# Performance work log

Measured on AMD Instinct MI355X. Metric: run time of the kernel, lower is better.

## Reference

```python
import jax, jax.numpy as jnp
import numpy as np
from functools import partial

MAX_SPAN_WIDTH = 8


def setup_inputs() -> dict:
    key = jax.random.key(0)
    ks = jax.random.split(key, 8)
    B, S, H = 4, 256, 256
    NE, D = 50000, 256  # entity_embedding_dim == hidden_size
    inp = {
        "embeddings": jax.random.normal(ks[0], (B, S, H), jnp.float32),          # BERT outputs[0]
        "entity_table": jax.random.normal(ks[1], (NE, D), jnp.float32) * 0.02,   # nn.Embedding weight
        "span_W": jax.random.normal(ks[2], (2 * H + 1, H), jnp.float32) * 0.02,  # span_embedding Linear
        "span_b": jax.random.normal(ks[3], (H,), jnp.float32) * 0.02,
        "gcn_W1": jax.random.normal(ks[4], (D, H), jnp.float32) * 0.02,
        "gcn_b1": jax.random.normal(ks[5], (H,), jnp.float32) * 0.02,
        "gcn_W2": jax.random.normal(ks[6], (H, H), jnp.float32) * 0.02,
        "gcn_b2": jax.random.normal(ks[7], (H,), jnp.float32) * 0.02,
        "k": 8,
    }
    return inp


def _star_adj_norm(k, dtype):
    # k-node star graph (node 0 hub) with self-loops, symmetric GCN normalization
    A = jnp.zeros((k, k), dtype).at[0, 1:].set(1.0).at[1:, 0].set(1.0) + jnp.eye(k, dtype=dtype)
    deg = A.sum(axis=1)
    return A / jnp.sqrt(deg[:, None] * deg[None, :])


def reference(embeddings, entity_table, span_W, span_b, gcn_W1, gcn_b1, gcn_W2, gcn_b2, k):
    B, S, H = embeddings.shape
    Wmax = MAX_SPAN_WIDTH
    dtype = embeddings.dtype

    # token_inputs: CLS embedding per example
    cls = embeddings[:, 0, :]  # [B, H]

    # Vectorized ragged span max-pool: running max over widths 1..Wmax.
    # span_max[w, b, s, :] = max(embeddings[b, s : s+w+1, :])
    neg_inf = jnp.array(-jnp.inf, dtype)
    maxes = []
    cur = embeddings
    maxes.append(cur)
    for w in range(1, Wmax):
        shifted = jnp.concatenate(
            [embeddings[:, w:, :], jnp.full((B, w, H), neg_inf, dtype)], axis=1)
        cur = jnp.maximum(cur, shifted)  # -inf pad => out-of-range positions ignored
        maxes.append(cur)
    span_max = jnp.stack(maxes, axis=0)  # [Wmax, B, S, H]

    # concat(max-pool, CLS, span width) -> span_embedding Linear
    cls_b = jnp.broadcast_to(cls[None, :, None, :], (Wmax, B, S, H))
    width_feat = jnp.broadcast_to(
        jnp.arange(1, Wmax + 1, dtype=dtype)[:, None, None, None], (Wmax, B, S, 1))
    span_inputs = jnp.concatenate([span_max, cls_b, width_feat], axis=-1)  # [Wmax,B,S,2H+1]
    span_inputs = span_inputs.reshape(Wmax * B * S, 2 * H + 1)             # [N, 2H+1]
    span_repr = span_inputs @ span_W + span_b                              # [N, H]

    # build_subgraph: top-k similar entities per span (memory-bound similarity + top-k)
    sims = span_repr @ entity_table.T          # [N, NE]  ~1.6GB intermediate
    _, topk_idx = jax.lax.top_k(sims, k)       # [N, k]
    node_x = entity_table[topk_idx]            # gather -> [N, k, D]

    # 2-layer GCN on the fixed star subgraph (gather-linear-scatter equivalent)
    A_norm = _star_adj_norm(k, dtype)          # [k, k]
    h = jax.nn.relu(jnp.einsum('ij,njd,dh->nih', A_norm, node_x, gcn_W1) + gcn_b1)
    subgraph_out = jnp.einsum('ij,njd,dh->nih', A_norm, h, gcn_W2) + gcn_b2  # [N, k, H]

    return cls, span_repr, subgraph_out
```

## Files before the change

### kernel.cpp

```cpp
#include <hip/hip_runtime.h>

typedef unsigned short u16;
typedef unsigned int   u32;
typedef unsigned long long u64;
typedef short bf16x8 __attribute__((ext_vector_type(8)));
typedef float f32x4  __attribute__((ext_vector_type(4)));

#define INF_F __builtin_inff()

__device__ __forceinline__ u16 f2bf(float f) {
  u32 u = __float_as_uint(f);
  return (u16)((u + 0x7FFFu + ((u >> 16) & 1u)) >> 16);
}

__device__ __forceinline__ u32 sortf(float f) {
  u32 u = __float_as_uint(f);
  return u ^ ((u32)((int)u >> 31) | 0x80000000u);
}
__device__ __forceinline__ float unsortf(u32 s) {
  u32 u = s ^ ((s & 0x80000000u) ? 0x80000000u : 0xFFFFFFFFu);
  return __uint_as_float(u);
}
__device__ __forceinline__ u64 sx64(u64 v, int m) {
  u32 lo = __shfl_xor((u32)v, m);
  u32 hi = __shfl_xor((u32)(v >> 32), m);
  return ((u64)hi << 32) | lo;
}

__device__ __forceinline__ void gload_lds16(const void* g, void* l) {
  __builtin_amdgcn_global_load_lds(
      (const __attribute__((address_space(1))) u32*)g,
      (__attribute__((address_space(3))) u32*)l, 16, 0, 0);
}

__global__ __launch_bounds__(256) void k0_cvt(
    const float* __restrict__ src, u16* __restrict__ dst, int n4) {
  int id = blockIdx.x * 256 + threadIdx.x;
  if (id >= n4) return;
  float4 v = ((const float4*)src)[id];
  ((ushort4*)dst)[id] = make_ushort4(f2bf(v.x), f2bf(v.y), f2bf(v.z), f2bf(v.w));
}

__global__ __launch_bounds__(256) void k1_span(
    const float* __restrict__ emb, const float* __restrict__ Wsp,
    const float* __restrict__ bsp,
    float* __restrict__ out0, float* __restrict__ out1,
    u16* __restrict__ spanbf) {
  __shared__ float SM[8][256];
  __shared__ float CLS[256];
  const int bid = blockIdx.x;
  const int b = bid >> 8, s = bid & 255;
  const int t = threadIdx.x;
  const float* eb = emb + (size_t)b * 65536;

  CLS[t] = eb[t];
  if (s == 0) out0[b * 256 + t] = eb[t];

  float m = eb[s * 256 + t];
  SM[0][t] = m;
  #pragma unroll
  for (int w = 1; w < 8; ++w) {
    if (s + w < 256) m = fmaxf(m, eb[(s + w) * 256 + t]);
    SM[w][t] = m;
  }
  __syncthreads();

  float cc = 0.f;
  for (int k = 0; k < 256; k += 4) {
    float4 cq = *(const float4*)&CLS[k];
    cc += cq.x * Wsp[(size_t)(256 + k + 0) * 256 + t];
    cc += cq.y * Wsp[(size_t)(256 + k + 1) * 256 + t];
    cc += cq.z * Wsp[(size_t)(256 + k + 2) * 256 + t];
    cc += cq.w * Wsp[(size_t)(256 + k + 3) * 256 + t];
  }
  float acc[8];
  const float base = bsp[t] + cc;
  #pragma unroll
  for (int w = 0; w < 8; ++w) acc[w] = base;

  for (int k = 0; k < 256; k += 4) {
    float w0 = Wsp[(size_t)(k + 0) * 256 + t];
    float w1 = Wsp[(size_t)(k + 1) * 256 + t];
    float w2 = Wsp[(size_t)(k + 2) * 256 + t];
    float w3 = Wsp[(size_t)(k + 3) * 256 + t];
    #pragma unroll
    for (int w = 0; w < 8; ++w) {
      float4 smq = *(const float4*)&SM[w][k];
      acc[w] += smq.x * w0; acc[w] += smq.y * w1;
      acc[w] += smq.z * w2; acc[w] += smq.w * w3;
    }
  }
  const float wm = Wsp[(size_t)512 * 256 + t];
  #pragma unroll
  for (int w = 0; w < 8; ++w) {
    float val = acc[w] + (float)(w + 1) * wm;
    size_t idx = ((size_t)w * 1024 + bid) * 256 + t;
    out1[idx] = val;
    spanbf[idx] = f2bf(val);
  }
}

__global__ __launch_bounds__(128) void k2_mfma(
    const u16* __restrict__ spanbf, const u16* __restrict__ entbf, int ne,
    float* __restrict__ Rpv, int* __restrict__ Rpi) {
  __shared__ u32 Elds[8192];
  __shared__ u64 Q[2][64][17];
  const int t = threadIdx.x, lane = t & 63, wv = t >> 6;
  const int m = lane & 15, q = lane >> 4, q4 = q * 4;
  const int p = blockIdx.x & 7, rg = blockIdx.x >> 3;
  const int psz = (ne + 7) >> 3;
  const int e_start = p * psz;
  const int e_end = min(ne, e_start + psz);
  const int rowbase = rg * 128 + wv * 64;
  const u64 gm = 0xFFFFull << (q * 16);
  const u64 lanelow = (lane == 63) ? 0x7FFFFFFFFFFFFFFFull
                                   : ((1ull << (lane + 1)) - 1) >> 1;
  const u64 gml = gm & lanelow;
  const int row = lane & 15;
  const int ls5 = lane >> 5;

  const u64 KINIT = ((u64)sortf(-INF_F) << 32);
  u64 slot[4][4];
  float myth[4], th[4][4];
  #pragma unroll
  for (int h = 0; h < 4; ++h) {
    myth[h] = -INF_F;
    #pragma unroll
    for (int s = 0; s < 4; ++s) { slot[h][s] = KINIT; th[h][s] = -INF_F; }
  }

  bf16x8 a[4][8];
  #pragma unroll
  for (int h = 0; h < 4; ++h)
    #pragma unroll
    for (int s = 0; s < 8; ++s)
      a[h][s] = *(const bf16x8*)(spanbf
                  + (size_t)(rowbase + h * 16 + m) * 256 + s * 32 + q * 8);

  auto issue = [&](int c, int ebase) {
    #pragma unroll
    for (int i = 0; i < 4; ++i) {
      int e = c * 16 + wv * 8 + i * 2 + ls5;
      int ge = min(ebase + e, e_end - 1);
      int xoff = ((lane & 31) ^ (e & 31)) << 4;
      const char* src = (const char*)entbf + (size_t)ge * 512 + xoff;
      char* dst = (char*)Elds + (c << 13) + (wv << 12) + (i << 10);
      gload_lds16(src, dst);
    }
  };

  const int ntiles = (e_end - e_start + 63) >> 6;
  #pragma unroll
  for (int c = 0; c < 4; ++c) issue(c, e_start);

  for (int tile = 0; tile < ntiles; ++tile) {
    const int eb = e_start + (tile << 6);
    const int ebn = eb + 64;
    const bool notlast = (tile + 1 < ntiles);
    #pragma unroll
    for (int c = 0; c < 4; ++c) {
      if (notlast) asm volatile("s_waitcnt vmcnt(12)" ::: "memory");
      else         asm volatile("s_waitcnt vmcnt(0)"  ::: "memory");
      __builtin_amdgcn_sched_barrier(0);
      __builtin_amdgcn_s_barrier();

      f32x4 acc[4];
      #pragma unroll
      for (int h = 0; h < 4; ++h) acc[h] = (f32x4){0.f, 0.f, 0.f, 0.f};
      const int el = c * 16 + m, sw = el & 31, bc = el << 5;
      #pragma unroll
      for (int s = 0; s < 8; ++s) {
        int qq = s * 4 + q;
        bf16x8 bfr = *(const bf16x8*)((const char*)Elds + ((bc | (qq ^ sw)) << 4));
        #pragma unroll
        for (int h = 0; h < 4; ++h)
          acc[h] = __builtin_amdgcn_mfma_f32_16x16x32_bf16(a[h][s], bfr, acc[h], 0, 0, 0);
      }
      const int gent = eb + c * 16 + m;
      const bool valid = gent < e_end;

      #pragma unroll
      for (int h = 0; h < 4; ++h) {
        bool any = valid & ((acc[h][0] > th[h][0]) | (acc[h][1] > th[h][1]) |
                            (acc[h][2] > th[h][2]) | (acc[h][3] > th[h][3]));
        if (!__ballot(any)) continue;
        u64 M[4];
        #pragma unroll
        for (int r = 0; r < 4; ++r) {
          bool hr = valid && (acc[h][r] > th[h][r]);
          M[r] = __ballot(hr);
          if (hr) {
            int pos = (int)__popcll(M[r] & gml);
            Q[wv][h * 16 + q4 + r][pos] =
                ((u64)sortf(acc[h][r]) << 32) | (u32)(~(u32)gent);
          }
        }
        u64 msk = (row & 2) ? ((row & 1) ? M[3] : M[2])
                            : ((row & 1) ? M[1] : M[0]);
        int cnt = (int)__popcll((msk >> ((row >> 2) << 4)) & 0xFFFFull);
        int cmax = cnt;
        #pragma unroll
        for (int o = 1; o < 16; o <<= 1)
          cmax = max(cmax, __shfl_xor(cmax, o));
        for (int j = 0; j < cmax; ++j) {
          u64 cand = Q[wv][h * 16 + row][j];
          if (j >= cnt) cand = 0;
          u64 m01 = slot[h][0] < slot[h][1] ? slot[h][0] : slot[h][1];
          u64 m23 = slot[h][2] < slot[h][3] ? slot[h][2] : slot[h][3];
          u64 lmin = m01 < m23 ? m01 : m23;
          u64 g = sx64(lmin, 16); if (g < lmin) lmin = g;
          g = sx64(lmin, 32); u64 gmin = (g < lmin) ? g : lmin;
          bool ins = cand > gmin;
          #pragma unroll
          for (int s2 = 0; s2 < 4; ++s2)
            if (ins && slot[h][s2] == gmin) slot[h][s2] = cand;
        }
        {
          u64 m01 = slot[h][0] < slot[h][1] ? slot[h][0] : slot[h][1];
          u64 m23 = slot[h][2] < slot[h][3] ? slot[h][2] : slot[h][3];
          u64 lmin = m01 < m23 ? m01 : m23;
          u64 g = sx64(lmin, 16); if (g < lmin) lmin = g;
          g = sx64(lmin, 32); if (g < lmin) lmin = g;
          myth[h] = unsortf((u32)(lmin >> 32));
          #pragma unroll
          for (int r = 0; r < 4; ++r) th[h][r] = __shfl(myth[h], q4 + r);
        }
      }

      __builtin_amdgcn_s_barrier();
      if (notlast) issue(c, ebn);
    }
  }

  {
    const int sg = lane >> 4;
    #pragma unroll
    for (int h = 0; h < 4; ++h) {
      int r0 = rowbase + h * 16 + row;
      #pragma unroll
      for (int s = 0; s < 4; ++s) {
        u64 e0 = slot[h][s];
        int col = p * 16 + sg * 4 + s;
        Rpv[(size_t)r0 * 128 + col] = unsortf((u32)(e0 >> 32));
        Rpi[(size_t)r0 * 128 + col] = (int)(~(u32)e0);
      }
    }
  }
}

__global__ __launch_bounds__(256) void k2_merge(
    const float* __restrict__ Rpv, const int* __restrict__ Rpi,
    int* __restrict__ Ridx) {
  const int t = threadIdx.x, lane = t & 63, wv = t >> 6;
  const int row = blockIdx.x * 4 + wv;
  const float va = Rpv[(size_t)row * 128 + lane];
  const int   ea = Rpi[(size_t)row * 128 + lane];
  const float vb = Rpv[(size_t)row * 128 + 64 + lane];
  const int   eb = Rpi[(size_t)row * 128 + 64 + lane];
  int ca = 0, cb = 0;
  for (int i = 0; i < 64; ++i) {
    float ov = __shfl(va, i); int oi = __shfl(ea, i);
    ca += (ov > va || (ov == va && oi < ea));
    cb += (ov > vb || (ov == vb && oi < eb));
  }
  for (int i = 0; i < 64; ++i) {
    float ov = __shfl(vb, i); int oi = __shfl(eb, i);
    ca += (ov > va || (ov == va && oi < ea));
    cb += (ov > vb || (ov == vb && oi < eb));
  }
  if (ca < 16) Ridx[(size_t)row * 16 + ca] = ea;
  if (cb < 16) Ridx[(size_t)row * 16 + cb] = eb;
}

__global__ __launch_bounds__(256, 3) void k3_gcn(
    const float* __restrict__ out1, const float* __restrict__ ent,
    const int* __restrict__ Ridx,
    const float* __restrict__ W1, const float* __restrict__ b1,
    const float* __restrict__ W2, const float* __restrict__ b2,
    float* __restrict__ out2, int ne) {
  __shared__ __align__(16) char UN[34560];
  __shared__ __align__(16) u16 Abf[32][272];
  __shared__ int cidx[4][16];
  __shared__ int chos[4][8];
  const int t = threadIdx.x;
  const int lane = t & 63, wv = t >> 6;
  const int m = lane & 15, q = lane >> 4;
  const int n0 = blockIdx.x * 4;

  {
    float  (*SPR)[256] = (float (*)[256])UN;
    double (*dpart)[4] = (double (*)[4])(UN + 4096);
    double (*sims)[16] = (double (*)[16])(UN + 6144);
    #pragma unroll
    for (int g = 0; g < 4; ++g)
      SPR[g][t] = out1[(size_t)(n0 + g) * 256 + t];
    if (t < 64) {
      int g = t >> 4, j = t & 15;
      int c = Ridx[(size_t)(n0 + g) * 16 + j];
      if ((unsigned)c >= (unsigned)ne) c = 0;
      cidx[g][j] = c;
    }
    __syncthreads();

    {
      const int pr = t >> 2, sub = t & 3;
      const int g = pr >> 4, j = pr & 15;
      const float* er = ent + (size_t)cidx[g][j] * 256 + sub * 64;
      const float* sr = &SPR[g][sub * 64];
      double s = 0.0;
      #pragma unroll
      for (int i = 0; i < 64; i += 4) {
        float4 e4 = *(const float4*)&er[i];
        float4 s4 = *(const float4*)&sr[i];
        s += (double)e4.x * (double)s4.x;
        s += (double)e4.y * (double)s4.y;
        s += (double)e4.z * (double)s4.z;
        s += (double)e4.w * (double)s4.w;
      }
      dpart[pr][sub] = s;
    }
    __syncthreads();
    if (t < 64) {
      int g = t >> 4, j = t & 15;
      sims[g][j] = dpart[t][0] + dpart[t][1] + dpart[t][2] + dpart[t][3];
    }
    __syncthreads();
    if (t < 4) {
      unsigned used = 0;
      for (int o = 0; o < 8; ++o) {
        int best = -1; double bv = 0.0; int bi = 0;
        for (int j = 0; j < 16; ++j) {
          if (used & (1u << j)) continue;
          if (best < 0 || sims[t][j] > bv || (sims[t][j] == bv && cidx[t][j] < bi)) {
            best = j; bv = sims[t][j]; bi = cidx[t][j];
          }
        }
        used |= (1u << best);
        chos[t][o] = cidx[t][best];
      }
    }
    __syncthreads();
  }

  {
    const int r = t >> 3, cb = t & 7;
    const float* src = ent + (size_t)chos[r >> 3][r & 7] * 256 + cb * 32;
    u32 pk[16];
    #pragma unroll
    for (int i = 0; i < 8; ++i) {
      float4 v = *(const float4*)&src[i * 4];
      pk[2 * i]     = (u32)f2bf(v.x) | ((u32)f2bf(v.y) << 16);
      pk[2 * i + 1] = (u32)f2bf(v.z) | ((u32)f2bf(v.w) << 16);
    }
    uint4* dst = (uint4*)&Abf[r][cb * 32];
    #pragma unroll
    for (int i = 0; i < 4; ++i)
      dst[i] = make_uint4(pk[4 * i], pk[4 * i + 1], pk[4 * i + 2], pk[4 * i + 3]);
  }

  auto run_gemm = [&](const float* __restrict__ Wg) {
    f32x4 acc[2][4];
    #pragma unroll
    for (int mt = 0; mt < 2; ++mt)
      #pragma unroll
      for (int nt = 0; nt < 4; ++nt)
        acc[mt][nt] = (f32x4){0.f, 0.f, 0.f, 0.f};

    for (int s = 0; s < 8; ++s) {
      __syncthreads();
      {
        const float* src = Wg + (size_t)(s * 32) * 256 + t;
        u32 pk[16];
        #pragma unroll
        for (int i = 0; i < 16; ++i) {
          float lo = src[(size_t)(2 * i) * 256];
          float hi = src[(size_t)(2 * i + 1) * 256];
          pk[i] = (u32)f2bf(lo) | ((u32)f2bf(hi) << 16);
        }
        uint4* dst = (uint4*)(UN + t * 80);
        #pragma unroll
        for (int i = 0; i < 4; ++i)
          dst[i] = make_uint4(pk[4 * i], pk[4 * i + 1], pk[4 * i + 2], pk[4 * i + 3]);
      }
      __syncthreads();
      #pragma unroll
      for (int mt = 0; mt < 2; ++mt) {
        bf16x8 af = *(const bf16x8*)((const char*)Abf
                       + (mt * 16 + m) * 544 + s * 64 + q * 16);
        #pragma unroll
        for (int nt = 0; nt < 4; ++nt) {
          const int col = wv * 64 + nt * 16 + m;
          bf16x8 bf = *(const bf16x8*)(UN + col * 80 + q * 16);
          acc[mt][nt] = __builtin_amdgcn_mfma_f32_16x16x32_bf16(
              af, bf, acc[mt][nt], 0, 0, 0);
        }
      }
    }
    __syncthreads();
    #pragma unroll
    for (int mt = 0; mt < 2; ++mt)
      #pragma unroll
      for (int nt = 0; nt < 4; ++nt)
        #pragma unroll
        for (int r = 0; r < 4; ++r)
          *(float*)(UN + (((mt * 16 + q * 4 + r) * 268)
                          + (wv * 64 + nt * 16 + m)) * 4) = acc[mt][nt][r];
    __syncthreads();
  };

  run_gemm(W1);
  {
    const float bb = b1[t];
    #pragma unroll
    for (int g = 0; g < 4; ++g) {
      float v[8];
      #pragma unroll
      for (int j = 0; j < 8; ++j)
        v[j] = *(const float*)(UN + ((g * 8 + j) * 268 + t) * 4);
      float ssum = 0.f;
      #pragma unroll
      for (int j = 1; j < 8; ++j) ssum += v[j];
      Abf[g * 8][t] = f2bf(fmaxf(v[0] * 0.125f + ssum * 0.25f + bb, 0.f));
      #pragma unroll
      for (int j = 1; j < 8; ++j)
        Abf[g * 8 + j][t] = f2bf(fmaxf(v[0] * 0.25f + v[j] * 0.5f + bb, 0.f));
    }
  }

  run_gemm(W2);
  {
    const float bb = b2[t];
    #pragma unroll
    for (int g = 0; g < 4; ++g) {
      float v[8];
      #pragma unroll
      for (int j = 0; j < 8; ++j)
        v[j] = *(const float*)(UN + ((g * 8 + j) * 268 + t) * 4);
      float ssum = 0.f;
      #pragma unroll
      for (int j = 1; j < 8; ++j) ssum += v[j];
      float* ob = out2 + (size_t)(n0 + g) * 2048 + t;
      ob[0] = v[0] * 0.125f + ssum * 0.25f + bb;
      #pragma unroll
      for (int j = 1; j < 8; ++j)
        ob[(size_t)j * 256] = v[0] * 0.25f + v[j] * 0.5f + bb;
    }
  }
}

extern "C" void kernel_launch(void* const* d_in, const int* in_sizes, int n_in,
                              void* d_out, int out_size, void* d_ws, size_t ws_size,
                              hipStream_t stream) {
  const float* emb = (const float*)d_in[0];
  const float* ent = (const float*)d_in[1];
  const float* Wsp = (const float*)d_in[2];
  const float* bsp = (const float*)d_in[3];
  const float* W1  = (const float*)d_in[4];
  const float* b1  = (const float*)d_in[5];
  const float* W2  = (const float*)d_in[6];
  const float* b2  = (const float*)d_in[7];
  const int ne = in_sizes[1] / 256;

  float* out  = (float*)d_out;
  float* out0 = out;
  float* out1 = out + 1024;
  float* out2 = out + 1024 + 2097152;

  char* ov = (char*)out2;
  u16*   entbf  = (u16*)(ov);
  u16*   spanbf = (u16*)(ov + 33554432);
  float* Rpv    = (float*)(ov + 41943040);
  int*   Rpi    = (int*)  (ov + 50331648);
  int*   Ridx   = (int*)d_ws;

  hipLaunchKernelGGL(k0_cvt, dim3((ne * 64 + 255) / 256), dim3(256), 0, stream,
                     ent, entbf, ne * 64);
  hipLaunchKernelGGL(k1_span, dim3(1024), dim3(256), 0, stream,
                     emb, Wsp, bsp, out0, out1, spanbf);
  hipLaunchKernelGGL(k2_mfma, dim3(512), dim3(128), 0, stream,
                     spanbf, entbf, ne, Rpv, Rpi);
  hipLaunchKernelGGL(k2_merge, dim3(2048), dim3(256), 0, stream,
                     Rpv, Rpi, Ridx);
  hipLaunchKernelGGL(k3_gcn, dim3(2048), dim3(256), 0, stream,
                     out1, ent, Ridx, W1, b1, W2, b2, out2, ne);
}
```

Baseline: 883.1 us.

## Split entity range 16-way and use 3-slot rolling chunk pipeline in top-k kernel

Doubles the entity partitions per row group (16 instead of 8), launching 1024 blocks so more waves run concurrently on the GPU, and the merge kernel now merges 256 partial candidates per row. The load pipeline changes from 4-chunk tiles with a trailing barrier to a 3-slot rolling buffer that prefetches one chunk ahead, shrinking LDS use to allow 2 blocks per CU. The candidate queue padding is replaced with XOR swizzling to avoid bank conflicts. It adds merge work, plus extra partial-result traffic and slot-maintenance overhead per partition.

```diff
diff --git a/kernel.cpp b/kernel.cpp
--- a/kernel.cpp
+++ b/kernel.cpp
@@ -100,15 +100,15 @@
   }
 }
 
-__global__ __launch_bounds__(128) void k2_mfma(
+__global__ __launch_bounds__(128, 2) void k2_mfma(
     const u16* __restrict__ spanbf, const u16* __restrict__ entbf, int ne,
     float* __restrict__ Rpv, int* __restrict__ Rpi) {
-  __shared__ u32 Elds[8192];
-  __shared__ u64 Q[2][64][17];
+  __shared__ u32 Elds[6144];
+  __shared__ u64 Q[2][64][16];
   const int t = threadIdx.x, lane = t & 63, wv = t >> 6;
   const int m = lane & 15, q = lane >> 4, q4 = q * 4;
-  const int p = blockIdx.x & 7, rg = blockIdx.x >> 3;
-  const int psz = (ne + 7) >> 3;
+  const int p = blockIdx.x & 15, rg = blockIdx.x >> 4;
+  const int psz = (ne + 15) >> 4;
   const int e_start = p * psz;
   const int e_end = min(ne, e_start + psz);
   const int rowbase = rg * 128 + wv * 64;
@@ -137,99 +137,97 @@
       a[h][s] = *(const bf16x8*)(spanbf
                   + (size_t)(rowbase + h * 16 + m) * 256 + s * 32 + q * 8);
 
-  auto issue = [&](int c, int ebase) {
+  auto issue = [&](int k, int sl) {
+    const int cb = e_start + (k << 4);
     #pragma unroll
     for (int i = 0; i < 4; ++i) {
-      int e = c * 16 + wv * 8 + i * 2 + ls5;
-      int ge = min(ebase + e, e_end - 1);
+      int eo = wv * 8 + i * 2 + ls5;
+      int e  = (sl << 4) + eo;
+      int ge = min(cb + eo, e_end - 1);
       int xoff = ((lane & 31) ^ (e & 31)) << 4;
-      const char* src = (const char*)entbf + (size_t)ge * 512 + xoff;
-      char* dst = (char*)Elds + (c << 13) + (wv << 12) + (i << 10);
-      gload_lds16(src, dst);
+      gload_lds16((const char*)entbf + (size_t)ge * 512 + xoff,
+                  (char*)Elds + (sl << 13) + (wv << 12) + (i << 10));
     }
   };
 
-  const int ntiles = (e_end - e_start + 63) >> 6;
-  #pragma unroll
-  for (int c = 0; c < 4; ++c) issue(c, e_start);
-
-  for (int tile = 0; tile < ntiles; ++tile) {
-    const int eb = e_start + (tile << 6);
-    const int ebn = eb + 64;
-    const bool notlast = (tile + 1 < ntiles);
-    #pragma unroll
-    for (int c = 0; c < 4; ++c) {
-      if (notlast) asm volatile("s_waitcnt vmcnt(12)" ::: "memory");
-      else         asm volatile("s_waitcnt vmcnt(0)"  ::: "memory");
-      __builtin_amdgcn_sched_barrier(0);
-      __builtin_amdgcn_s_barrier();
-
-      f32x4 acc[4];
-      #pragma unroll
-      for (int h = 0; h < 4; ++h) acc[h] = (f32x4){0.f, 0.f, 0.f, 0.f};
-      const int el = c * 16 + m, sw = el & 31, bc = el << 5;
-      #pragma unroll
-      for (int s = 0; s < 8; ++s) {
-        int qq = s * 4 + q;
-        bf16x8 bfr = *(const bf16x8*)((const char*)Elds + ((bc | (qq ^ sw)) << 4));
-        #pragma unroll
-        for (int h = 0; h < 4; ++h)
-          acc[h] = __builtin_amdgcn_mfma_f32_16x16x32_bf16(a[h][s], bfr, acc[h], 0, 0, 0);
-      }
-      const int gent = eb + c * 16 + m;
-      const bool valid = gent < e_end;
-
-      #pragma unroll
-      for (int h = 0; h < 4; ++h) {
-        bool any = valid & ((acc[h][0] > th[h][0]) | (acc[h][1] > th[h][1]) |
-                            (acc[h][2] > th[h][2]) | (acc[h][3] > th[h][3]));
-        if (!__ballot(any)) continue;
-        u64 M[4];
-        #pragma unroll
-        for (int r = 0; r < 4; ++r) {
-          bool hr = valid && (acc[h][r] > th[h][r]);
-          M[r] = __ballot(hr);
-          if (hr) {
-            int pos = (int)__popcll(M[r] & gml);
-            Q[wv][h * 16 + q4 + r][pos] =
-                ((u64)sortf(acc[h][r]) << 32) | (u32)(~(u32)gent);
-          }
+  const int nch = (e_end - e_start + 15) >> 4;
+  int cs = 0;
+  issue(0, 0);
+
+  for (int pc = 0; pc < nch; ++pc) {
+    int is_ = cs + 1; if (is_ == 3) is_ = 0;
+    if (pc + 1 < nch) {
+      issue(pc + 1, is_);
+      asm volatile("s_waitcnt vmcnt(4)" ::: "memory");
+    } else {
+      asm volatile("s_waitcnt vmcnt(0)" ::: "memory");
+    }
+    __builtin_amdgcn_sched_barrier(0);
+    __builtin_amdgcn_s_barrier();
+
+    f32x4 acc[4];
+    #pragma unroll
+    for (int h = 0; h < 4; ++h) acc[h] = (f32x4){0.f, 0.f, 0.f, 0.f};
+    const int el = (cs << 4) + m, sw = el & 31, bc = el << 5;
+    #pragma unroll
+    for (int s = 0; s < 8; ++s) {
+      int qq = s * 4 + q;
+      bf16x8 bfr = *(const bf16x8*)((const char*)Elds + ((bc | (qq ^ sw)) << 4));
+      #pragma unroll
+      for (int h = 0; h < 4; ++h)
+        acc[h] = __builtin_amdgcn_mfma_f32_16x16x32_bf16(a[h][s], bfr, acc[h], 0, 0, 0);
+    }
+    const int gent = e_start + (pc << 4) + m;
+    const bool valid = gent < e_end;
+
+    #pragma unroll
+    for (int h = 0; h < 4; ++h) {
+      bool any = valid & ((acc[h][0] > th[h][0]) | (acc[h][1] > th[h][1]) |
+                          (acc[h][2] > th[h][2]) | (acc[h][3] > th[h][3]));
+      if (!__ballot(any)) continue;
+      u64 M[4];
+      #pragma unroll
+      for (int r = 0; r < 4; ++r) {
+        bool hr = valid && (acc[h][r] > th[h][r]);
+        M[r] = __ballot(hr);
+        if (hr) {
+          int pos = (int)__popcll(M[r] & gml);
+          Q[wv][h * 16 + q4 + r][pos ^ (q4 + r)] =
+              ((u64)sortf(acc[h][r]) << 32) | (u32)(~(u32)gent);
         }
-        u64 msk = (row & 2) ? ((row & 1) ? M[3] : M[2])
-                            : ((row & 1) ? M[1] : M[0]);
-        int cnt = (int)__popcll((msk >> ((row >> 2) << 4)) & 0xFFFFull);
-        int cmax = cnt;
-        #pragma unroll
-        for (int o = 1; o < 16; o <<= 1)
-          cmax = max(cmax, __shfl_xor(cmax, o));
-        for (int j = 0; j < cmax; ++j) {
-          u64 cand = Q[wv][h * 16 + row][j];
-          if (j >= cnt) cand = 0;
-          u64 m01 = slot[h][0] < slot[h][1] ? slot[h][0] : slot[h][1];
-          u64 m23 = slot[h][2] < slot[h][3] ? slot[h][2] : slot[h][3];
-          u64 lmin = m01 < m23 ? m01 : m23;
-          u64 g = sx64(lmin, 16); if (g < lmin) lmin = g;
-          g = sx64(lmin, 32); u64 gmin = (g < lmin) ? g : lmin;
-          bool ins = cand > gmin;
-          #pragma unroll
-          for (int s2 = 0; s2 < 4; ++s2)
-            if (ins && slot[h][s2] == gmin) slot[h][s2] = cand;
-        }
-        {
-          u64 m01 = slot[h][0] < slot[h][1] ? slot[h][0] : slot[h][1];
-          u64 m23 = slot[h][2] < slot[h][3] ? slot[h][2] : slot[h][3];
-          u64 lmin = m01 < m23 ? m01 : m23;
-          u64 g = sx64(lmin, 16); if (g < lmin) lmin = g;
-          g = sx64(lmin, 32); if (g < lmin) lmin = g;
-          myth[h] = unsortf((u32)(lmin >> 32));
-          #pragma unroll
-          for (int r = 0; r < 4; ++r) th[h][r] = __shfl(myth[h], q4 + r);
-        }
-      }
-
-      __builtin_amdgcn_s_barrier();
-      if (notlast) issue(c, ebn);
-    }
+      }
+      u64 msk = (row & 2) ? ((row & 1) ? M[3] : M[2])
+                          : ((row & 1) ? M[1] : M[0]);
+      int cnt = (int)__popcll((msk >> ((row >> 2) << 4)) & 0xFFFFull);
+      int cmax = cnt;
+      #pragma unroll
+      for (int o = 1; o < 16; o <<= 1)
+        cmax = max(cmax, __shfl_xor(cmax, o));
+      for (int j = 0; j < cmax; ++j) {
+        u64 cand = Q[wv][h * 16 + row][j ^ row];
+        if (j >= cnt) cand = 0;
+        u64 m01 = slot[h][0] < slot[h][1] ? slot[h][0] : slot[h][1];
+        u64 m23 = slot[h][2] < slot[h][3] ? slot[h][2] : slot[h][3];
+        u64 lmin = m01 < m23 ? m01 : m23;
+        u64 g = sx64(lmin, 16); if (g < lmin) lmin = g;
+        g = sx64(lmin, 32); u64 gmin = (g < lmin) ? g : lmin;
+        bool ins = cand > gmin;
+        #pragma unroll
+        for (int s2 = 0; s2 < 4; ++s2)
+          if (ins && slot[h][s2] == gmin) slot[h][s2] = cand;
+      }
+      {
+        u64 m01 = slot[h][0] < slot[h][1] ? slot[h][0] : slot[h][1];
+        u64 m23 = slot[h][2] < slot[h][3] ? slot[h][2] : slot[h][3];
+        u64 lmin = m01 < m23 ? m01 : m23;
+        u64 g = sx64(lmin, 16); if (g < lmin) lmin = g;
+        g = sx64(lmin, 32); if (g < lmin) lmin = g;
+        myth[h] = unsortf((u32)(lmin >> 32));
+        #pragma unroll
+        for (int r = 0; r < 4; ++r) th[h][r] = __shfl(myth[h], q4 + r);
+      }
+    }
+    cs = is_;
   }
 
   {
@@ -241,8 +239,8 @@
       for (int s = 0; s < 4; ++s) {
         u64 e0 = slot[h][s];
         int col = p * 16 + sg * 4 + s;
-        Rpv[(size_t)r0 * 128 + col] = unsortf((u32)(e0 >> 32));
-        Rpi[(size_t)r0 * 128 + col] = (int)(~(u32)e0);
+        Rpv[(size_t)r0 * 256 + col] = unsortf((u32)(e0 >> 32));
+        Rpi[(size_t)r0 * 256 + col] = (int)(~(u32)e0);
       }
     }
   }
@@ -253,23 +251,25 @@
     int* __restrict__ Ridx) {
   const int t = threadIdx.x, lane = t & 63, wv = t >> 6;
   const int row = blockIdx.x * 4 + wv;
-  const float va = Rpv[(size_t)row * 128 + lane];
-  const int   ea = Rpi[(size_t)row * 128 + lane];
-  const float vb = Rpv[(size_t)row * 128 + 64 + lane];
-  const int   eb = Rpi[(size_t)row * 128 + 64 + lane];
-  int ca = 0, cb = 0;
-  for (int i = 0; i < 64; ++i) {
-    float ov = __shfl(va, i); int oi = __shfl(ea, i);
-    ca += (ov > va || (ov == va && oi < ea));
-    cb += (ov > vb || (ov == vb && oi < eb));
-  }
-  for (int i = 0; i < 64; ++i) {
-    float ov = __shfl(vb, i); int oi = __shfl(eb, i);
-    ca += (ov > va || (ov == va && oi < ea));
-    cb += (ov > vb || (ov == vb && oi < eb));
-  }
-  if (ca < 16) Ridx[(size_t)row * 16 + ca] = ea;
-  if (cb < 16) Ridx[(size_t)row * 16 + cb] = eb;
+  float v[4]; int e[4];
+  #pragma unroll
+  for (int pg = 0; pg < 4; ++pg) {
+    v[pg] = Rpv[(size_t)row * 256 + pg * 64 + lane];
+    e[pg] = Rpi[(size_t)row * 256 + pg * 64 + lane];
+  }
+  int c[4] = {0, 0, 0, 0};
+  #pragma unroll
+  for (int ps = 0; ps < 4; ++ps) {
+    for (int i = 0; i < 64; ++i) {
+      float ov = __shfl(v[ps], i); int oi = __shfl(e[ps], i);
+      #pragma unroll
+      for (int pd = 0; pd < 4; ++pd)
+        c[pd] += (ov > v[pd] || (ov == v[pd] && oi < e[pd]));
+    }
+  }
+  #pragma unroll
+  for (int pg = 0; pg < 4; ++pg)
+    if (c[pg] < 16) Ridx[(size_t)row * 16 + c[pg]] = e[pg];
 }
 
 __global__ __launch_bounds__(256, 3) void k3_gcn(
@@ -477,7 +477,7 @@
                      ent, entbf, ne * 64);
   hipLaunchKernelGGL(k1_span, dim3(1024), dim3(256), 0, stream,
                      emb, Wsp, bsp, out0, out1, spanbf);
-  hipLaunchKernelGGL(k2_mfma, dim3(512), dim3(128), 0, stream,
+  hipLaunchKernelGGL(k2_mfma, dim3(1024), dim3(128), 0, stream,
                      spanbf, entbf, ne, Rpv, Rpi);
   hipLaunchKernelGGL(k2_merge, dim3(2048), dim3(256), 0, stream,
                      Rpv, Rpi, Ridx);
```

Result: faster. 739.5 us (-16.3%).
